# Performance work log

Measured on AMD Instinct MI355X. Metric: run time of the kernel, lower is better.

## Reference

```python
import jax, jax.numpy as jnp
import numpy as np

D = 64            # node_out_feats
G = 1000          # number of graphs in batch
NPG = 32          # nodes per graph
N = G * NPG       # total nodes = 32000
E = 80000         # total edges
NODE_IN = 74
EDGE_IN = 12
EH = 128          # edge_hidden_feats
STEPS_MP = 6
STEPS_S2S = 6
LSTM_LAYERS = 3
N_TASKS = 1


def setup_inputs() -> dict:
    key = jax.random.key(0)
    ks = jax.random.split(key, 32)

    def lin(k, fi, fo):
        return (jax.random.normal(k, (fi, fo), jnp.float32) / np.float32(np.sqrt(fi)))

    # edges constrained within graphs
    eg = jax.random.randint(ks[0], (E,), 0, G)
    inp = {
        "node_feats": jax.random.normal(ks[1], (N, NODE_IN), jnp.float32),
        "edge_feats": jax.random.normal(ks[2], (E, EDGE_IN), jnp.float32),
        "src": (eg * NPG + jax.random.randint(ks[3], (E,), 0, NPG)).astype(jnp.int32),
        "dst": (eg * NPG + jax.random.randint(ks[4], (E,), 0, NPG)).astype(jnp.int32),
        "segment_ids": (jnp.arange(N, dtype=jnp.int32) // NPG),
        "Wp": lin(ks[5], NODE_IN, D), "bp": jnp.zeros((D,), jnp.float32),
        "We1": lin(ks[6], EDGE_IN, EH), "be1": jnp.zeros((EH,), jnp.float32),
        "We2": lin(ks[7], EH, D * D), "be2": jnp.zeros((D * D,), jnp.float32),
        "b_conv": jnp.zeros((D,), jnp.float32),
        "gru_Wx": lin(ks[8], D, 3 * D), "gru_Wh": lin(ks[9], D, 3 * D),
        "gru_bx": jnp.zeros((3 * D,), jnp.float32), "gru_bh": jnp.zeros((3 * D,), jnp.float32),
        "Wout1": lin(ks[10], 2 * D, D), "bout1": jnp.zeros((D,), jnp.float32),
        "Wout2": lin(ks[11], D, N_TASKS), "bout2": jnp.zeros((N_TASKS,), jnp.float32),
    }
    for l in range(LSTM_LAYERS):
        fi = 2 * D if l == 0 else D
        inp[f"lstm_Wx{l}"] = lin(ks[12 + 4 * l], fi, 4 * D)
        inp[f"lstm_Wh{l}"] = lin(ks[13 + 4 * l], D, 4 * D)
        inp[f"lstm_bx{l}"] = jnp.zeros((4 * D,), jnp.float32)
        inp[f"lstm_bh{l}"] = jnp.zeros((4 * D,), jnp.float32)
    return inp


def reference(node_feats, edge_feats, src, dst, segment_ids,
              Wp, bp, We1, be1, We2, be2, b_conv,
              gru_Wx, gru_Wh, gru_bx, gru_bh,
              Wout1, bout1, Wout2, bout2,
              lstm_Wx0, lstm_Wh0, lstm_bx0, lstm_bh0,
              lstm_Wx1, lstm_Wh1, lstm_bx1, lstm_bh1,
              lstm_Wx2, lstm_Wh2, lstm_bx2, lstm_bh2):
    # ---- MPNNGNN ----
    h = jax.nn.relu(node_feats @ Wp + bp)                 # [N, D]
    hidden = h                                            # GRU hidden state
    # edge network -> per-edge [D, D] weight matrix (edge feats are constant,
    # so compute once; DGL recomputes each step with identical result)
    W_edge = (jax.nn.relu(edge_feats @ We1 + be1) @ We2 + be2).reshape(E, D, D)
    for _ in range(STEPS_MP):
        msg = jnp.einsum('ed,edo->eo', h[src], W_edge)    # [E, D] per-edge matvec
        agg = jax.ops.segment_sum(msg, dst, num_segments=N) + b_conv
        x = jax.nn.relu(agg)
        # GRU cell (torch gate order r, z, n)
        gx = x @ gru_Wx + gru_bx
        gh = hidden @ gru_Wh + gru_bh
        r = jax.nn.sigmoid(gx[:, :D] + gh[:, :D])
        z = jax.nn.sigmoid(gx[:, D:2 * D] + gh[:, D:2 * D])
        n = jnp.tanh(gx[:, 2 * D:] + r * gh[:, 2 * D:])
        hidden = (1.0 - z) * n + z * hidden
        h = hidden
    # ---- Set2Set readout ----
    lstm = [(lstm_Wx0, lstm_Wh0, lstm_bx0, lstm_bh0),
            (lstm_Wx1, lstm_Wh1, lstm_bx1, lstm_bh1),
            (lstm_Wx2, lstm_Wh2, lstm_bx2, lstm_bh2)]
    hs = [jnp.zeros((G, D), h.dtype) for _ in range(LSTM_LAYERS)]
    cs = [jnp.zeros((G, D), h.dtype) for _ in range(LSTM_LAYERS)]
    q_star = jnp.zeros((G, 2 * D), h.dtype)
    for _ in range(STEPS_S2S):
        xq = q_star
        for l, (Wx, Wh, bx, bh) in enumerate(lstm):
            gates = xq @ Wx + bx + hs[l] @ Wh + bh        # [G, 4D], torch order i,f,g,o
            i, f, g_, o = jnp.split(gates, 4, axis=-1)
            c = jax.nn.sigmoid(f) * cs[l] + jax.nn.sigmoid(i) * jnp.tanh(g_)
            hs[l] = jax.nn.sigmoid(o) * jnp.tanh(c)
            cs[l] = c
            xq = hs[l]
        q = xq                                            # [G, D]
        e = jnp.sum(h * q[segment_ids], axis=-1)          # [N] attention logits
        emax = jax.ops.segment_max(e, segment_ids, num_segments=G)
        ee = jnp.exp(e - emax[segment_ids])
        alpha = ee / jax.ops.segment_sum(ee, segment_ids, num_segments=G)[segment_ids]
        readout = jax.ops.segment_sum(h * alpha[:, None], segment_ids, num_segments=G)
        q_star = jnp.concatenate([q, readout], axis=-1)   # [G, 2D]
    # ---- prediction head ----
    pred = jax.nn.relu(q_star @ Wout1 + bout1) @ Wout2 + bout2
    return pred, q_star
```

## Files before the change

kernel.cpp:

```cpp
#include <hip/hip_runtime.h>

typedef __attribute__((ext_vector_type(8))) _Float16 f16x8;
typedef __attribute__((ext_vector_type(2))) _Float16 f16x2;
typedef __attribute__((ext_vector_type(4))) float floatx4;

union HFrag { uint4 u4; f16x8 v; unsigned short s[8]; };
union HS { _Float16 h; unsigned short u; };
union UH2 { unsigned int u; f16x2 h; };

__device__ __forceinline__ float bf2f(unsigned short u) {
  return __uint_as_float(((unsigned int)u) << 16);
}
__device__ __forceinline__ float h2f(unsigned short u) { HS z; z.u = u; return (float)z.h; }
__device__ __forceinline__ unsigned short f2h(float f) { HS z; z.h = (_Float16)f; return z.u; }
__device__ __forceinline__ float sigmf(float x) { return 1.0f / (1.0f + expf(-x)); }

__device__ __forceinline__ float ldi(const void* p, long i, bool f32) {
  return f32 ? ((const float*)p)[i] : bf2f(((const unsigned short*)p)[i]);
}

__device__ __forceinline__ void dma16(unsigned short* lds, const unsigned short* g) {
  __builtin_amdgcn_global_load_lds(
      (const __attribute__((address_space(1))) unsigned int*)g,
      (__attribute__((address_space(3))) unsigned int*)lds,
      16, 0, 0);
}

#define WAIT_VM5()   __builtin_amdgcn_s_waitcnt(0x0F75)
#define WAIT_VM0()   __builtin_amdgcn_s_waitcnt(0x0F70)
#define WAIT_LGKM0() __builtin_amdgcn_s_waitcnt(0xC07F)

#define SAFE_BARRIER() do {                      \
  __builtin_amdgcn_sched_barrier(0);             \
  WAIT_LGKM0();                                  \
  __builtin_amdgcn_s_barrier();                  \
  __builtin_amdgcn_sched_barrier(0);             \
} while (0)

#define NNODES 32000
#define NEDGES 80000
#define NGRAPH 1000

#define MFMA_F16 __builtin_amdgcn_mfma_f32_16x16x32_f16

__global__ __launch_bounds__(256) void detect_kernel(
    const unsigned short* __restrict__ nf, int* __restrict__ flag) {
  __shared__ float sm[256];
  float m = 0.f;
  for (int i = threadIdx.x; i < 4096; i += 256) {
    float v = fabsf(bf2f(nf[i]));
    if (isfinite(v)) m = fmaxf(m, v);
    else m = 1e30f;
  }
  sm[threadIdx.x] = m;
  __syncthreads();
  if (threadIdx.x == 0) {
    float mm = 0.f;
    for (int i = 0; i < 256; ++i) mm = fmaxf(mm, sm[i]);
    flag[0] = (mm > 1e6f) ? 1 : 0;
  }
}

__global__ __launch_bounds__(256) void prep_kernel(
    const int* __restrict__ dflag,
    const void* __restrict__ Wx, const void* __restrict__ Wh,
    const void* __restrict__ bx, const void* __restrict__ bh,
    const void* __restrict__ bconv,
    unsigned short* __restrict__ WxH, unsigned short* __restrict__ WhH,
    float* __restrict__ bxf, float* __restrict__ bhf, float* __restrict__ bconvf) {
  bool f32 = dflag[0] != 0;
  int idx = blockIdx.x * 256 + threadIdx.x;
  int j = idx >> 6, k = idx & 63;
  WxH[idx] = f2h(ldi(Wx, k * 192 + j, f32));
  WhH[idx] = f2h(ldi(Wh, k * 192 + j, f32));
  if (idx < 192) { bxf[idx] = ldi(bx, idx, f32); bhf[idx] = ldi(bh, idx, f32); }
  if (idx < 64) bconvf[idx] = ldi(bconv, idx, f32);
}

__global__ __launch_bounds__(256) void lstmprep_kernel(
    const int* __restrict__ dflag,
    const void* Wx0, const void* Wh0, const void* bx0, const void* bh0,
    const void* Wx1, const void* Wh1, const void* bx1, const void* bh1,
    const void* Wx2, const void* Wh2, const void* bx2, const void* bh2,
    float4* __restrict__ LW, float* __restrict__ bsum) {
  bool f32 = dflag[0] != 0;
  int idx = blockIdx.x * 256 + threadIdx.x;
  int l, base, fi;
  if (idx < 12288)      { l = 0; base = 0;     fi = 128; }
  else if (idx < 20480) { l = 1; base = 12288; fi = 64; }
  else                  { l = 2; base = 20480; fi = 64; }
  const void* Wx = (l == 0) ? Wx0 : (l == 1) ? Wx1 : Wx2;
  const void* Wh = (l == 0) ? Wh0 : (l == 1) ? Wh1 : Wh2;
  int r = idx - base;
  int c = r >> 8, t = r & 255;
  float v[4];
#pragma unroll
  for (int i2 = 0; i2 < 4; ++i2) {
    int k = c * 4 + i2;
    v[i2] = (k < fi) ? ldi(Wx, (long)k * 256 + t, f32)
                     : ldi(Wh, (long)(k - fi) * 256 + t, f32);
  }
  float4 o; o.x = v[0]; o.y = v[1]; o.z = v[2]; o.w = v[3];
  LW[idx] = o;
  if (idx < 768) {
    int ll = idx >> 8, j = idx & 255;
    const void* bx = (ll == 0) ? bx0 : (ll == 1) ? bx1 : bx2;
    const void* bh = (ll == 0) ? bh0 : (ll == 1) ? bh1 : bh2;
    bsum[idx] = ldi(bx, j, f32) + ldi(bh, j, f32);
  }
}

__global__ __launch_bounds__(256) void nodeproj_kernel(
    const int* __restrict__ dflag,
    const void* __restrict__ nf, const void* __restrict__ Wp,
    const void* __restrict__ bp, float* __restrict__ hstate) {
  bool f32 = dflag[0] != 0;
  int lane = threadIdx.x & 63;
  int n = blockIdx.x * 4 + (threadIdx.x >> 6);
  float acc = ldi(bp, lane, f32);
  for (int k = 0; k < 74; ++k)
    acc += ldi(nf, (long)n * 74 + k, f32) * ldi(Wp, k * 64 + lane, f32);
  hstate[n * 64 + lane] = fmaxf(acc, 0.0f);
}

__global__ __launch_bounds__(256) void we2t_kernel(
    const int* __restrict__ dflag,
    const void* __restrict__ We2, unsigned short* __restrict__ We2T) {
  bool f32 = dflag[0] != 0;
  int idx = blockIdx.x * 256 + threadIdx.x;
  int j = idx & 7;
  int gs = (idx >> 3) & 7;
  int o = (idx >> 6) & 63;
  int k = idx >> 12;
  int g = gs ^ (o & 7);
  int d = g * 8 + j;
  We2T[idx] = f2h(ldi(We2, (long)k * 4096 + d * 64 + o, f32));
}

__global__ __launch_bounds__(256) void be2t_kernel(
    const int* __restrict__ dflag,
    const void* __restrict__ be2, unsigned short* __restrict__ be2T) {
  bool f32 = dflag[0] != 0;
  int idx = blockIdx.x * 256 + threadIdx.x;
  int j = idx & 7;
  int gs = (idx >> 3) & 7;
  int o = idx >> 6;
  int g = gs ^ (o & 7);
  int d = g * 8 + j;
  be2T[idx] = f2h(ldi(be2, (long)d * 64 + o, f32));
}

__global__ __launch_bounds__(256) void count_kernel(
    const int* __restrict__ dst, int* __restrict__ cnt) {
  int e = blockIdx.x * 256 + threadIdx.x;
  if (e < NEDGES) atomicAdd(&cnt[dst[e]], 1);
}

__global__ __launch_bounds__(256) void scan_kernel(
    const int* __restrict__ cnt, int* __restrict__ row_ptr, int* __restrict__ cur) {
  __shared__ int part[256];
  int t = threadIdx.x;
  int base = t * 125;
  int s = 0;
  for (int i = 0; i < 125; ++i) s += cnt[base + i];
  part[t] = s;
  __syncthreads();
  if (t == 0) {
    int run = 0;
    for (int i = 0; i < 256; ++i) { int v = part[i]; part[i] = run; run += v; }
  }
  __syncthreads();
  int run = part[t];
  for (int i = 0; i < 125; ++i) {
    row_ptr[base + i] = run;
    cur[base + i] = run;
    run += cnt[base + i];
  }
  if (t == 255) row_ptr[32000] = run;
}

__global__ __launch_bounds__(256) void fill_kernel(
    const int* __restrict__ dst, int* __restrict__ cur, int* __restrict__ eidx) {
  int e = blockIdx.x * 256 + threadIdx.x;
  if (e < NEDGES) { int p = atomicAdd(&cur[dst[e]], 1); eidx[p] = e; }
}

__global__ __launch_bounds__(256) void uprep_kernel(
    const int* __restrict__ dflag,
    const void* __restrict__ ef, const void* __restrict__ We1,
    const void* __restrict__ be1, const int* __restrict__ eidx,
    unsigned int* __restrict__ uT) {
  bool f32 = dflag[0] != 0;
  __shared__ float we1_s[1536];
  __shared__ float be1_s[128];
  int t = threadIdx.x;
  for (int i = t; i < 1536; i += 256) we1_s[i] = ldi(We1, i, f32);
  if (t < 128) be1_s[t] = ldi(be1, t, f32);
  __syncthreads();
  int pos = blockIdx.x * 256 + t;
  if (pos >= NEDGES) return;
  int e = eidx[pos];
  float efr[12];
#pragma unroll
  for (int j = 0; j < 12; ++j) efr[j] = ldi(ef, (long)e * 12 + j, f32);
#pragma unroll 4
  for (int kp = 0; kp < 64; ++kp) {
    int k0 = kp * 2;
    float u0 = be1_s[k0], u1 = be1_s[k0 + 1];
#pragma unroll
    for (int j = 0; j < 12; ++j) {
      u0 += efr[j] * we1_s[j * 128 + k0];
      u1 += efr[j] * we1_s[j * 128 + k0 + 1];
    }
    u0 = fmaxf(u0, 0.f); u1 = fmaxf(u1, 0.f);
    HS a, b; a.h = (_Float16)u0; b.h = (_Float16)u1;
    uT[(size_t)kp * NEDGES + pos] = (unsigned int)a.u | ((unsigned int)b.u << 16);
  }
}

__device__ __forceinline__ void issueB(unsigned short* L, const unsigned short* G,
                                       int w, int lane) {
  L += w * 1024; G += w * 1024 + lane * 8;
  dma16(L, G); dma16(L + 512, G + 512);
  dma16(L + 4096, G + 4096); dma16(L + 4096 + 512, G + 4096 + 512);
}

__device__ __forceinline__ void zchunk(
    unsigned short (*BtL)[8192], unsigned int (*Zs)[64][68],
    const HFrag (&bhi)[4][2], const HFrag (&blo)[4][2],
    int arow, int g0q, int g1q, int c16, int w, int q,
    int cb, int zc, bool act, int r, unsigned int ucur, floatx4 (&msgv)[16]) {
  HFrag a00, a01, a10, a11;
  a00.u4 = *(const uint4*)&BtL[cb][arow + g0q];
  a01.u4 = *(const uint4*)&BtL[cb][arow + g1q];
  a10.u4 = *(const uint4*)&BtL[cb][4096 + arow + g0q];
  a11.u4 = *(const uint4*)&BtL[cb][4096 + arow + g1q];
  __builtin_amdgcn_sched_barrier(0);
  WAIT_LGKM0();
  __builtin_amdgcn_sched_barrier(0);
  floatx4 z0[4], z1[4];
#pragma unroll
  for (int nt = 0; nt < 4; ++nt) {
    z0[nt] = (floatx4){0.f, 0.f, 0.f, 0.f};
    z1[nt] = (floatx4){0.f, 0.f, 0.f, 0.f};
  }
#pragma unroll
  for (int nt = 0; nt < 4; ++nt) {
    z0[nt] = MFMA_F16(a00.v, bhi[nt][0].v, z0[nt], 0, 0, 0);
    z0[nt] = MFMA_F16(a00.v, blo[nt][0].v, z0[nt], 0, 0, 0);
    z0[nt] = MFMA_F16(a01.v, bhi[nt][1].v, z0[nt], 0, 0, 0);
    z0[nt] = MFMA_F16(a01.v, blo[nt][1].v, z0[nt], 0, 0, 0);
    z1[nt] = MFMA_F16(a10.v, bhi[nt][0].v, z1[nt], 0, 0, 0);
    z1[nt] = MFMA_F16(a10.v, blo[nt][0].v, z1[nt], 0, 0, 0);
    z1[nt] = MFMA_F16(a11.v, bhi[nt][1].v, z1[nt], 0, 0, 0);
    z1[nt] = MFMA_F16(a11.v, blo[nt][1].v, z1[nt], 0, 0, 0);
  }
#pragma unroll
  for (int nt = 0; nt < 4; ++nt) {
    uint4 st;
    HS p0h, p1h;
    p0h.h = (_Float16)z0[nt][0]; p1h.h = (_Float16)z1[nt][0];
    st.x = (unsigned int)p0h.u | ((unsigned int)p1h.u << 16);
    p0h.h = (_Float16)z0[nt][1]; p1h.h = (_Float16)z1[nt][1];
    st.y = (unsigned int)p0h.u | ((unsigned int)p1h.u << 16);
    p0h.h = (_Float16)z0[nt][2]; p1h.h = (_Float16)z1[nt][2];
    st.z = (unsigned int)p0h.u | ((unsigned int)p1h.u << 16);
    p0h.h = (_Float16)z0[nt][3]; p1h.h = (_Float16)z1[nt][3];
    st.w = (unsigned int)p0h.u | ((unsigned int)p1h.u << 16);
    *(uint4*)&Zs[zc][nt * 16 + c16][w * 16 + q * 4] = st;
  }
  SAFE_BARRIER();
  if (act) {
    UH2 uu; uu.u = ucur;
#pragma unroll
    for (int og = 0; og < 16; ++og) {
      uint4 zz = *(const uint4*)&Zs[zc][r][og * 4];
      UH2 a;
      a.u = zz.x; msgv[og][0] = __builtin_amdgcn_fdot2(a.h, uu.h, msgv[og][0], false);
      a.u = zz.y; msgv[og][1] = __builtin_amdgcn_fdot2(a.h, uu.h, msgv[og][1], false);
      a.u = zz.z; msgv[og][2] = __builtin_amdgcn_fdot2(a.h, uu.h, msgv[og][2], false);
      a.u = zz.w; msgv[og][3] = __builtin_amdgcn_fdot2(a.h, uu.h, msgv[og][3], false);
    }
  }
}

__global__ __launch_bounds__(256, 2) void step_fused_kernel(
    const unsigned short* __restrict__ We2T,
    const unsigned short* __restrict__ be2T,
    const unsigned int* __restrict__ uT,
    const int* __restrict__ src, const int* __restrict__ eidx,
    const int* __restrict__ row_ptr,
    const unsigned short* __restrict__ WxH, const unsigned short* __restrict__ WhH,
    const float* __restrict__ bxf, const float* __restrict__ bhf,
    const float* __restrict__ bconvf,
    float* __restrict__ hstate) {
  __shared__ __align__(16) unsigned char RA[67584];
  unsigned short (*BtL)[8192] = (unsigned short (*)[8192])RA;
  unsigned int (*Zs)[64][68] = (unsigned int (*)[64][68])(RA + 32768);
  float (*MS)[64] = (float (*)[64])RA;
  unsigned short (*Xhi)[72] = (unsigned short (*)[72])RA;
  unsigned short (*Xlo)[72] = (unsigned short (*)[72])(RA + 9216);
  unsigned short (*SRZ)[65] = (unsigned short (*)[65])(RA + 18432);
  float (*NG)[65] = (float (*)[65])(RA + 35072);

  int t = threadIdx.x, lane = t & 63, w = t >> 6;
  int c16 = lane & 15, q = lane >> 4;
  int nb = blockIdx.x * 64;
  int p0 = row_ptr[nb], p1 = row_ptr[nb + 64];
  int nE = p1 - p0;

  HFrag bhi[4][2], blo[4][2];
#pragma unroll
  for (int nt = 0; nt < 4; ++nt)
#pragma unroll
    for (int ks = 0; ks < 2; ++ks) {
      const float* hp = hstate + (size_t)(nb + nt * 16 + c16) * 64 + ks * 32 + q * 8;
      float4 v0 = *(const float4*)hp;
      float4 v1 = *(const float4*)(hp + 4);
      float vv[8] = {v0.x, v0.y, v0.z, v0.w, v1.x, v1.y, v1.z, v1.w};
#pragma unroll
      for (int j = 0; j < 8; ++j) {
        HS hi; hi.h = (_Float16)vv[j];
        bhi[nt][ks].s[j] = hi.u;
        blo[nt][ks].s[j] = f2h(vv[j] - (float)hi.h);
      }
    }

  int arow = (w * 16 + c16) * 64;
  int g0q = (q ^ (c16 & 7)) * 8;
  int g1q = ((4 + q) ^ (c16 & 7)) * 8;

  float aggv[16];
  {
    float bcv = bconvf[lane];
#pragma unroll
    for (int i = 0; i < 16; ++i) aggv[i] = bcv;
  }

  for (int et = 0; et < nE; et += 256) {
    int me = et + t;
    bool act = me < nE;
    int pos = p0 + (act ? me : 0);
    int r = src[eidx[pos]] - nb;

    unsigned int uA = uT[pos];
    dma16(&BtL[0][0] + w * 1024, be2T + w * 1024 + lane * 8);
    dma16(&BtL[0][0] + w * 1024 + 512, be2T + w * 1024 + 512 + lane * 8);
    issueB(&BtL[1][0], We2T, w, lane);
    WAIT_VM0();

    floatx4 hacc[4];
#pragma unroll
    for (int nt = 0; nt < 4; ++nt) hacc[nt] = (floatx4){0.f, 0.f, 0.f, 0.f};
    {
      HFrag aB0, aB1;
      aB0.u4 = *(const uint4*)&BtL[0][arow + g0q];
      aB1.u4 = *(const uint4*)&BtL[0][arow + g1q];
#pragma unroll
      for (int nt = 0; nt < 4; ++nt) {
        hacc[nt] = MFMA_F16(aB0.v, bhi[nt][0].v, hacc[nt], 0, 0, 0);
        hacc[nt] = MFMA_F16(aB0.v, blo[nt][0].v, hacc[nt], 0, 0, 0);
        hacc[nt] = MFMA_F16(aB1.v, bhi[nt][1].v, hacc[nt], 0, 0, 0);
        hacc[nt] = MFMA_F16(aB1.v, blo[nt][1].v, hacc[nt], 0, 0, 0);
      }
    }
    __builtin_amdgcn_sched_barrier(0);
    WAIT_LGKM0();
    __builtin_amdgcn_sched_barrier(0);
    unsigned int uB = uT[(size_t)NEDGES + pos];
    issueB(&BtL[0][0], We2T + 8192, w, lane);
#pragma unroll
    for (int nt = 0; nt < 4; ++nt)
      *(floatx4*)&Zs[1][nt * 16 + c16][w * 16 + q * 4] = hacc[nt];
    SAFE_BARRIER();

    floatx4 msgv[16];
    if (act) {
#pragma unroll
      for (int og = 0; og < 16; ++og)
        msgv[og] = *(const floatx4*)&Zs[1][r][og * 4];
    }

    for (int cc = 0; cc < 32; ++cc) {
      const int c0 = cc * 2;
      WAIT_VM5();
      zchunk(BtL, Zs, bhi, blo, arow, g0q, g1q, c16, w, q, 1, 0, act, r, uA, msgv);
      if (c0 + 2 < 64) {
        __builtin_amdgcn_sched_barrier(0);
        uA = uT[(size_t)(c0 + 2) * NEDGES + pos];
        issueB(&BtL[1][0], We2T + (size_t)(c0 + 2) * 8192, w, lane);
      }
      if (c0 + 1 == 63) WAIT_VM0(); else WAIT_VM5();
      zchunk(BtL, Zs, bhi, blo, arow, g0q, g1q, c16, w, q, 0, 1, act, r, uB, msgv);
      if (c0 + 3 < 64) {
        __builtin_amdgcn_sched_barrier(0);
        uB = uT[(size_t)(c0 + 3) * NEDGES + pos];
        issueB(&BtL[0][0], We2T + (size_t)(c0 + 3) * 8192, w, lane);
      }
    }

    __syncthreads();
    if (act) {
      int t7 = t & 7;
#pragma unroll
      for (int og = 0; og < 16; ++og)
        *(floatx4*)&MS[t][(og ^ t7) * 4] = msgv[og];
    }
    __syncthreads();
    {
      int nT = nE - et; if (nT > 256) nT = 256;
      int c = t & 63;
      int cq = c >> 2, cj = c & 3;
#pragma unroll
      for (int i = 0; i < 16; ++i) {
        int node = nb + (t >> 6) + i * 4;
        int rs = row_ptr[node] - p0 - et;
        int re = row_ptr[node + 1] - p0 - et;
        int lo = rs < 0 ? 0 : rs;
        int hi = re > nT ? nT : re;
        float a = aggv[i];
        for (int p = lo; p < hi; ++p)
          a += MS[p][((cq ^ (p & 7)) << 2) | cj];
        aggv[i] = a;
      }
    }
    __syncthreads();
  }

#pragma unroll
  for (int i = 0; i < 16; ++i) {
    int n = (t >> 6) + i * 4;
    int c = t & 63;
    float x = fmaxf(aggv[i], 0.f);
    HS hx; hx.h = (_Float16)x;
    Xhi[n][c] = hx.u;
    Xlo[n][c] = f2h(x - (float)hx.h);
  }
  __syncthreads();

  floatx4 gx[3][4], gh[3][4];
#pragma unroll
  for (int jt = 0; jt < 3; ++jt)
#pragma unroll
    for (int nt = 0; nt < 4; ++nt) {
      gx[jt][nt] = (floatx4){0.f, 0.f, 0.f, 0.f};
      gh[jt][nt] = (floatx4){0.f, 0.f, 0.f, 0.f};
    }
#pragma unroll
  for (int kc = 0; kc < 2; ++kc) {
    int kof = kc * 32 + q * 8;
    HFrag ax[3], ah[3];
#pragma unroll
    for (int jt = 0; jt < 3; ++jt) {
      long off = (long)((w * 3 + jt) * 16 + c16) * 64 + kof;
      ax[jt].u4 = *(const uint4*)(WxH + off);
      ah[jt].u4 = *(const uint4*)(WhH + off);
    }
    HFrag bxh[4], bxl[4];
#pragma unroll
    for (int nt = 0; nt < 4; ++nt) {
      int n = nt * 16 + c16;
      bxh[nt].u4 = *(const uint4*)&Xhi[n][kof];
      bxl[nt].u4 = *(const uint4*)&Xlo[n][kof];
    }
#pragma unroll
    for (int jt = 0; jt < 3; ++jt)
#pragma unroll
      for (int nt = 0; nt < 4; ++nt) {
        gx[jt][nt] = MFMA_F16(ax[jt].v, bxh[nt].v, gx[jt][nt], 0, 0, 0);
        gx[jt][nt] = MFMA_F16(ax[jt].v, bxl[nt].v, gx[jt][nt], 0, 0, 0);
        gh[jt][nt] = MFMA_F16(ah[jt].v, bhi[nt][kc].v, gh[jt][nt], 0, 0, 0);
      }
  }

#pragma unroll
  for (int jt = 0; jt < 3; ++jt) {
#pragma unroll
    for (int rr = 0; rr < 4; ++rr) {
      int j = (w * 3 + jt) * 16 + q * 4 + rr;
      float bxv = bxf[j], bhv = bhf[j];
#pragma unroll
      for (int nt = 0; nt < 4; ++nt) {
        float vx = gx[jt][nt][rr] + bxv;
        float vh = gh[jt][nt][rr] + bhv;
        if (j < 128) {
          SRZ[j][nt * 16 + c16] = f2h(sigmf(vx + vh));
        } else {
          gx[jt][nt][rr] = vx;
          gh[jt][nt][rr] = vh;
        }
      }
    }
  }
  __syncthreads();

#pragma unroll
  for (int jt = 0; jt < 3; ++jt) {
#pragma unroll
    for (int rr = 0; rr < 4; ++rr) {
      int j = (w * 3 + jt) * 16 + q * 4 + rr;
      if (j >= 128) {
        int f = j - 128;
#pragma unroll
        for (int nt = 0; nt < 4; ++nt) {
          int n = nt * 16 + c16;
          float rg = h2f(SRZ[f][n]);
          NG[f][n] = tanhf(gx[jt][nt][rr] + rg * gh[jt][nt][rr]);
        }
      }
    }
  }
  __syncthreads();

#pragma unroll
  for (int i = 0; i < 16; ++i) {
    int n = (t >> 6) + i * 4;
    int f = t & 63;
    float z = h2f(SRZ[64 + f][n]);
    float ng = NG[f][n];
    size_t gi = (size_t)(nb + n) * 64 + f;
    float ho = hstate[gi];
    hstate[gi] = (1.0f - z) * ng + z * ho;
  }
}

__global__ __launch_bounds__(512) void s2s6_kernel(
    const int* __restrict__ dflag,
    const float* __restrict__ hstate,
    const float4* __restrict__ LW,
    const float* __restrict__ lstm_bsum,
    const void* __restrict__ Wout1, const void* __restrict__ bout1,
    const void* __restrict__ Wout2, const void* __restrict__ bout2,
    float* __restrict__ out) {
  bool f32 = dflag[0] != 0;
  __shared__ float xq[2][128];
  __shared__ float inb[2][192];
  __shared__ float gates[2][256];
  __shared__ float al[2][32];
  __shared__ float hsvf[384];
  __shared__ float csvf[384];
  int g0 = blockIdx.x * 2;
  int t = threadIdx.x;

  for (int i = t; i < 256; i += 512) xq[i >> 7][i & 127] = 0.f;
  for (int i = t; i < 384; i += 512) { hsvf[i] = 0.f; csvf[i] = 0.f; }
  __syncthreads();

  int tt = t & 255, gp = t >> 8;

  for (int s = 0; s < 6; ++s) {
#pragma unroll
    for (int l = 0; l < 3; ++l) {
      const int fi = (l == 0) ? 128 : 64;
      const int tot = fi + 64;
      for (int i = t; i < 2 * tot; i += 512) {
        int g = i / tot, k = i - g * tot;
        inb[g][k] = (k < fi) ? xq[g][k] : hsvf[l * 128 + g * 64 + (k - fi)];
      }
      __syncthreads();
      const int nch = tot >> 2;
      const float4* wrow = LW + ((l == 0) ? 0 : (l == 1) ? 12288 : 20480) + tt;
      float bs = lstm_bsum[l * 256 + tt];
      float a0 = bs;
#pragma unroll 8
      for (int cch = 0; cch < nch; ++cch) {
        float4 wv = wrow[(size_t)cch * 256];
        float4 x0 = *(const float4*)&inb[gp][cch * 4];
        a0 += wv.x * x0.x + wv.y * x0.y + wv.z * x0.z + wv.w * x0.w;
      }
      gates[gp][tt] = a0;
      __syncthreads();
      if (t < 128) {
        int gg = t >> 6, u = t & 63;
        float ig = sigmf(gates[gg][u]);
        float fg = sigmf(gates[gg][64 + u]);
        float gv = tanhf(gates[gg][128 + u]);
        float og = sigmf(gates[gg][192 + u]);
        int ci = l * 128 + t;
        float cc = fg * csvf[ci] + ig * gv;
        float hn = og * tanhf(cc);
        csvf[ci] = cc;
        hsvf[ci] = hn;
        xq[gg][u] = hn;
      }
      __syncthreads();
    }
    if (t < 128) {
      int gg = t >> 6, tl = t & 63;
      int g = g0 + gg;
      int n = tl & 31, half = tl >> 5;
      const float* hrow = hstate + (size_t)(g * 32 + n) * 64 + half * 32;
      const float* qp = &xq[gg][half * 32];
      float p = 0.f;
#pragma unroll
      for (int k = 0; k < 32; ++k) p += hrow[k] * qp[k];
      p += __shfl_xor(p, 32, 64);
      if (half == 0) {
        float m = p;
#pragma unroll
        for (int s2 = 1; s2 < 32; s2 <<= 1) m = fmaxf(m, __shfl_xor(m, s2, 32));
        float e = expf(p - m);
        float sum = e;
#pragma unroll
        for (int s2 = 1; s2 < 32; s2 <<= 1) sum += __shfl_xor(sum, s2, 32);
        al[gg][n] = e / sum;
      }
      float acc = 0.f;
#pragma unroll 8
      for (int nn = 0; nn < 32; ++nn)
        acc += al[gg][nn] * hstate[(size_t)(g * 32 + nn) * 64 + tl];
      xq[gg][64 + tl] = acc;
    }
    __syncthreads();
  }

  if (t < 128) {
    int gg = t >> 6, tl = t & 63;
    int g = g0 + gg;
    float acc = ldi(bout1, tl, f32);
#pragma unroll 16
    for (int k = 0; k < 128; ++k) acc += xq[gg][k] * ldi(Wout1, k * 64 + tl, f32);
    acc = fmaxf(acc, 0.0f);
    float p = acc * ldi(Wout2, tl, f32);
#pragma unroll
    for (int m = 1; m < 64; m <<= 1) p += __shfl_xor(p, m, 64);
    if (tl == 0) out[g] = p + ldi(bout2, 0, f32);
    out[1000 + g * 128 + tl] = xq[gg][tl];
    out[1000 + g * 128 + 64 + tl] = xq[gg][64 + tl];
  }
}

extern "C" void kernel_launch(void* const* d_in, const int* in_sizes, int n_in,
                              void* d_out, int out_size, void* d_ws, size_t ws_size,
                              hipStream_t stream) {
  (void)in_sizes; (void)n_in; (void)out_size; (void)ws_size;
  const void* node_feats = d_in[0];
  const void* edge_feats = d_in[1];
  const int* src = (const int*)d_in[2];
  const int* dst = (const int*)d_in[3];
  const void* Wp = d_in[5];
  const void* bp = d_in[6];
  const void* We1 = d_in[7];
  const void* be1 = d_in[8];
  const void* We2 = d_in[9];
  const void* be2 = d_in[10];
  const void* b_conv = d_in[11];
  const void* gWx = d_in[12];
  const void* gWh = d_in[13];
  const void* gbx = d_in[14];
  const void* gbh = d_in[15];
  const void* Wout1 = d_in[16];
  const void* bout1 = d_in[17];
  const void* Wout2 = d_in[18];
  const void* bout2 = d_in[19];

  int* dflag = (int*)d_ws;
  float* hstate = (float*)d_ws + 64;
  unsigned int* uT = (unsigned int*)(hstate + NNODES * 64);
  unsigned short* We2T = (unsigned short*)(uT + (size_t)NEDGES * 64);
  unsigned short* WxH = We2T + 524288;
  unsigned short* WhH = WxH + 12288;
  float* bxf = (float*)(WhH + 12288);
  float* bhf = bxf + 192;
  float* bconvf = bhf + 192;
  int* row_ptr = (int*)(bconvf + 64);
  int* cur = row_ptr + 32001;
  int* cnt = cur + 32000;
  int* eidx = cnt + 32000;
  uintptr_t lwp = (uintptr_t)(eidx + 80000);
  lwp = (lwp + 15) & ~(uintptr_t)15;
  float4* LWf = (float4*)lwp;
  float* lstm_bsum = (float*)(LWf + 28672);
  unsigned short* be2T = (unsigned short*)(lstm_bsum + 768);

  (void)hipMemsetAsync(cnt, 0, (size_t)NNODES * sizeof(int), stream);

  detect_kernel<<<1, 256, 0, stream>>>((const unsigned short*)node_feats, dflag);
  prep_kernel<<<48, 256, 0, stream>>>(dflag, gWx, gWh, gbx, gbh, b_conv,
                                      WxH, WhH, bxf, bhf, bconvf);
  nodeproj_kernel<<<NNODES / 4, 256, 0, stream>>>(dflag, node_feats, Wp, bp, hstate);
  we2t_kernel<<<2048, 256, 0, stream>>>(dflag, We2, We2T);
  be2t_kernel<<<16, 256, 0, stream>>>(dflag, be2, be2T);
  lstmprep_kernel<<<112, 256, 0, stream>>>(dflag,
      d_in[20], d_in[21], d_in[22], d_in[23],
      d_in[24], d_in[25], d_in[26], d_in[27],
      d_in[28], d_in[29], d_in[30], d_in[31],
      LWf, lstm_bsum);

  count_kernel<<<(NEDGES + 255) / 256, 256, 0, stream>>>(dst, cnt);
  scan_kernel<<<1, 256, 0, stream>>>(cnt, row_ptr, cur);
  fill_kernel<<<(NEDGES + 255) / 256, 256, 0, stream>>>(dst, cur, eidx);
  uprep_kernel<<<(NEDGES + 255) / 256, 256, 0, stream>>>(
      dflag, edge_feats, We1, be1, eidx, uT);

  for (int step = 0; step < 6; ++step) {
    step_fused_kernel<<<NNODES / 64, 256, 0, stream>>>(
        We2T, be2T, uT, src, eidx, row_ptr, WxH, WhH, bxf, bhf, bconvf, hstate);
  }
  s2s6_kernel<<<NGRAPH / 2, 512, 0, stream>>>(dflag, hstate,
      (const float4*)LWf, lstm_bsum,
      Wout1, bout1, Wout2, bout2, (float*)d_out);
}
```

Baseline: 1.097 ms.

## Single-buffer We2 chunks and halve MS staging to fit three blocks per CU

Replaces the double-buffered We2T chunk pipeline with one LDS buffer. Each chunk's fragments are read into registers before the next chunk's DMA is issued. The message staging buffer is split into two 128-edge halves, which cuts the shared-memory footprint from about 66KB to about 51KB, and launch bounds are raised to 3 blocks per CU. The aim is higher occupancy to hide latency, at the cost of exposing the full global-load latency each chunk (wait on vmcnt 0), extra barriers, and tighter register limits.

```diff
diff --git a/kernel.cpp b/kernel.cpp
--- a/kernel.cpp
+++ b/kernel.cpp
@@ -26,7 +26,6 @@
       16, 0, 0);
 }
 
-#define WAIT_VM5()   __builtin_amdgcn_s_waitcnt(0x0F75)
 #define WAIT_VM0()   __builtin_amdgcn_s_waitcnt(0x0F70)
 #define WAIT_LGKM0() __builtin_amdgcn_s_waitcnt(0xC07F)
 
@@ -225,66 +224,7 @@
   dma16(L + 4096, G + 4096); dma16(L + 4096 + 512, G + 4096 + 512);
 }
 
-__device__ __forceinline__ void zchunk(
-    unsigned short (*BtL)[8192], unsigned int (*Zs)[64][68],
-    const HFrag (&bhi)[4][2], const HFrag (&blo)[4][2],
-    int arow, int g0q, int g1q, int c16, int w, int q,
-    int cb, int zc, bool act, int r, unsigned int ucur, floatx4 (&msgv)[16]) {
-  HFrag a00, a01, a10, a11;
-  a00.u4 = *(const uint4*)&BtL[cb][arow + g0q];
-  a01.u4 = *(const uint4*)&BtL[cb][arow + g1q];
-  a10.u4 = *(const uint4*)&BtL[cb][4096 + arow + g0q];
-  a11.u4 = *(const uint4*)&BtL[cb][4096 + arow + g1q];
-  __builtin_amdgcn_sched_barrier(0);
-  WAIT_LGKM0();
-  __builtin_amdgcn_sched_barrier(0);
-  floatx4 z0[4], z1[4];
-#pragma unroll
-  for (int nt = 0; nt < 4; ++nt) {
-    z0[nt] = (floatx4){0.f, 0.f, 0.f, 0.f};
-    z1[nt] = (floatx4){0.f, 0.f, 0.f, 0.f};
-  }
-#pragma unroll
-  for (int nt = 0; nt < 4; ++nt) {
-    z0[nt] = MFMA_F16(a00.v, bhi[nt][0].v, z0[nt], 0, 0, 0);
-    z0[nt] = MFMA_F16(a00.v, blo[nt][0].v, z0[nt], 0, 0, 0);
-    z0[nt] = MFMA_F16(a01.v, bhi[nt][1].v, z0[nt], 0, 0, 0);
-    z0[nt] = MFMA_F16(a01.v, blo[nt][1].v, z0[nt], 0, 0, 0);
-    z1[nt] = MFMA_F16(a10.v, bhi[nt][0].v, z1[nt], 0, 0, 0);
-    z1[nt] = MFMA_F16(a10.v, blo[nt][0].v, z1[nt], 0, 0, 0);
-    z1[nt] = MFMA_F16(a11.v, bhi[nt][1].v, z1[nt], 0, 0, 0);
-    z1[nt] = MFMA_F16(a11.v, blo[nt][1].v, z1[nt], 0, 0, 0);
-  }
-#pragma unroll
-  for (int nt = 0; nt < 4; ++nt) {
-    uint4 st;
-    HS p0h, p1h;
-    p0h.h = (_Float16)z0[nt][0]; p1h.h = (_Float16)z1[nt][0];
-    st.x = (unsigned int)p0h.u | ((unsigned int)p1h.u << 16);
-    p0h.h = (_Float16)z0[nt][1]; p1h.h = (_Float16)z1[nt][1];
-    st.y = (unsigned int)p0h.u | ((unsigned int)p1h.u << 16);
-    p0h.h = (_Float16)z0[nt][2]; p1h.h = (_Float16)z1[nt][2];
-    st.z = (unsigned int)p0h.u | ((unsigned int)p1h.u << 16);
-    p0h.h = (_Float16)z0[nt][3]; p1h.h = (_Float16)z1[nt][3];
-    st.w = (unsigned int)p0h.u | ((unsigned int)p1h.u << 16);
-    *(uint4*)&Zs[zc][nt * 16 + c16][w * 16 + q * 4] = st;
-  }
-  SAFE_BARRIER();
-  if (act) {
-    UH2 uu; uu.u = ucur;
-#pragma unroll
-    for (int og = 0; og < 16; ++og) {
-      uint4 zz = *(const uint4*)&Zs[zc][r][og * 4];
-      UH2 a;
-      a.u = zz.x; msgv[og][0] = __builtin_amdgcn_fdot2(a.h, uu.h, msgv[og][0], false);
-      a.u = zz.y; msgv[og][1] = __builtin_amdgcn_fdot2(a.h, uu.h, msgv[og][1], false);
-      a.u = zz.z; msgv[og][2] = __builtin_amdgcn_fdot2(a.h, uu.h, msgv[og][2], false);
-      a.u = zz.w; msgv[og][3] = __builtin_amdgcn_fdot2(a.h, uu.h, msgv[og][3], false);
-    }
-  }
-}
-
-__global__ __launch_bounds__(256, 2) void step_fused_kernel(
+__global__ __launch_bounds__(256, 3) void step_fused_kernel(
     const unsigned short* __restrict__ We2T,
     const unsigned short* __restrict__ be2T,
     const unsigned int* __restrict__ uT,
@@ -294,9 +234,9 @@
     const float* __restrict__ bxf, const float* __restrict__ bhf,
     const float* __restrict__ bconvf,
     float* __restrict__ hstate) {
-  __shared__ __align__(16) unsigned char RA[67584];
-  unsigned short (*BtL)[8192] = (unsigned short (*)[8192])RA;
-  unsigned int (*Zs)[64][68] = (unsigned int (*)[64][68])(RA + 32768);
+  __shared__ __align__(16) unsigned char RA[51712];
+  unsigned short* BtL = (unsigned short*)RA;
+  unsigned int (*Zs)[64][68] = (unsigned int (*)[64][68])(RA + 16384);
   float (*MS)[64] = (float (*)[64])RA;
   unsigned short (*Xhi)[72] = (unsigned short (*)[72])RA;
   unsigned short (*Xlo)[72] = (unsigned short (*)[72])(RA + 9216);
@@ -343,32 +283,29 @@
     int pos = p0 + (act ? me : 0);
     int r = src[eidx[pos]] - nb;
 
-    unsigned int uA = uT[pos];
-    dma16(&BtL[0][0] + w * 1024, be2T + w * 1024 + lane * 8);
-    dma16(&BtL[0][0] + w * 1024 + 512, be2T + w * 1024 + 512 + lane * 8);
-    issueB(&BtL[1][0], We2T, w, lane);
+    unsigned int ucur = uT[pos];
+    dma16(BtL + w * 1024, be2T + w * 1024 + lane * 8);
+    dma16(BtL + w * 1024 + 512, be2T + w * 1024 + 512 + lane * 8);
     WAIT_VM0();
 
-    floatx4 hacc[4];
-#pragma unroll
-    for (int nt = 0; nt < 4; ++nt) hacc[nt] = (floatx4){0.f, 0.f, 0.f, 0.f};
-    {
-      HFrag aB0, aB1;
-      aB0.u4 = *(const uint4*)&BtL[0][arow + g0q];
-      aB1.u4 = *(const uint4*)&BtL[0][arow + g1q];
-#pragma unroll
-      for (int nt = 0; nt < 4; ++nt) {
-        hacc[nt] = MFMA_F16(aB0.v, bhi[nt][0].v, hacc[nt], 0, 0, 0);
-        hacc[nt] = MFMA_F16(aB0.v, blo[nt][0].v, hacc[nt], 0, 0, 0);
-        hacc[nt] = MFMA_F16(aB1.v, bhi[nt][1].v, hacc[nt], 0, 0, 0);
-        hacc[nt] = MFMA_F16(aB1.v, blo[nt][1].v, hacc[nt], 0, 0, 0);
-      }
-    }
+    HFrag eb0, eb1;
+    eb0.u4 = *(const uint4*)&BtL[arow + g0q];
+    eb1.u4 = *(const uint4*)&BtL[arow + g1q];
     __builtin_amdgcn_sched_barrier(0);
     WAIT_LGKM0();
     __builtin_amdgcn_sched_barrier(0);
-    unsigned int uB = uT[(size_t)NEDGES + pos];
-    issueB(&BtL[0][0], We2T + 8192, w, lane);
+    issueB(BtL, We2T, w, lane);
+
+    floatx4 hacc[4];
+#pragma unroll
+    for (int nt = 0; nt < 4; ++nt) hacc[nt] = (floatx4){0.f, 0.f, 0.f, 0.f};
+#pragma unroll
+    for (int nt = 0; nt < 4; ++nt) {
+      hacc[nt] = MFMA_F16(eb0.v, bhi[nt][0].v, hacc[nt], 0, 0, 0);
+      hacc[nt] = MFMA_F16(eb0.v, blo[nt][0].v, hacc[nt], 0, 0, 0);
+      hacc[nt] = MFMA_F16(eb1.v, bhi[nt][1].v, hacc[nt], 0, 0, 0);
+      hacc[nt] = MFMA_F16(eb1.v, blo[nt][1].v, hacc[nt], 0, 0, 0);
+    }
 #pragma unroll
     for (int nt = 0; nt < 4; ++nt)
       *(floatx4*)&Zs[1][nt * 16 + c16][w * 16 + q * 4] = hacc[nt];
@@ -381,26 +318,75 @@
         msgv[og] = *(const floatx4*)&Zs[1][r][og * 4];
     }
 
-    for (int cc = 0; cc < 32; ++cc) {
-      const int c0 = cc * 2;
-      WAIT_VM5();
-      zchunk(BtL, Zs, bhi, blo, arow, g0q, g1q, c16, w, q, 1, 0, act, r, uA, msgv);
-      if (c0 + 2 < 64) {
-        __builtin_amdgcn_sched_barrier(0);
-        uA = uT[(size_t)(c0 + 2) * NEDGES + pos];
-        issueB(&BtL[1][0], We2T + (size_t)(c0 + 2) * 8192, w, lane);
-      }
-      if (c0 + 1 == 63) WAIT_VM0(); else WAIT_VM5();
-      zchunk(BtL, Zs, bhi, blo, arow, g0q, g1q, c16, w, q, 0, 1, act, r, uB, msgv);
-      if (c0 + 3 < 64) {
-        __builtin_amdgcn_sched_barrier(0);
-        uB = uT[(size_t)(c0 + 3) * NEDGES + pos];
-        issueB(&BtL[0][0], We2T + (size_t)(c0 + 3) * 8192, w, lane);
-      }
+    for (int c = 0; c < 64; ++c) {
+      WAIT_VM0();
+      HFrag a00, a01, a10, a11;
+      a00.u4 = *(const uint4*)&BtL[arow + g0q];
+      a01.u4 = *(const uint4*)&BtL[arow + g1q];
+      a10.u4 = *(const uint4*)&BtL[4096 + arow + g0q];
+      a11.u4 = *(const uint4*)&BtL[4096 + arow + g1q];
+      __builtin_amdgcn_sched_barrier(0);
+      WAIT_LGKM0();
+      __builtin_amdgcn_sched_barrier(0);
+      unsigned int unext = 0;
+      if (c + 1 < 64) {
+        unext = uT[(size_t)(c + 1) * NEDGES + pos];
+        issueB(BtL, We2T + (size_t)(c + 1) * 8192, w, lane);
+      }
+      floatx4 z0[4], z1[4];
+#pragma unroll
+      for (int nt = 0; nt < 4; ++nt) {
+        z0[nt] = (floatx4){0.f, 0.f, 0.f, 0.f};
+        z1[nt] = (floatx4){0.f, 0.f, 0.f, 0.f};
+      }
+#pragma unroll
+      for (int nt = 0; nt < 4; ++nt) {
+        z0[nt] = MFMA_F16(a00.v, bhi[nt][0].v, z0[nt], 0, 0, 0);
+        z0[nt] = MFMA_F16(a00.v, blo[nt][0].v, z0[nt], 0, 0, 0);
+        z0[nt] = MFMA_F16(a01.v, bhi[nt][1].v, z0[nt], 0, 0, 0);
+        z0[nt] = MFMA_F16(a01.v, blo[nt][1].v, z0[nt], 0, 0, 0);
+        z1[nt] = MFMA_F16(a10.v, bhi[nt][0].v, z1[nt], 0, 0, 0);
+        z1[nt] = MFMA_F16(a10.v, blo[nt][0].v, z1[nt], 0, 0, 0);
+        z1[nt] = MFMA_F16(a11.v, bhi[nt][1].v, z1[nt], 0, 0, 0);
+        z1[nt] = MFMA_F16(a11.v, blo[nt][1].v, z1[nt], 0, 0, 0);
+      }
+      int zc = c & 1;
+#pragma unroll
+      for (int nt = 0; nt < 4; ++nt) {
+        uint4 st;
+        HS ph0, ph1;
+        ph0.h = (_Float16)z0[nt][0]; ph1.h = (_Float16)z1[nt][0];
+        st.x = (unsigned int)ph0.u | ((unsigned int)ph1.u << 16);
+        ph0.h = (_Float16)z0[nt][1]; ph1.h = (_Float16)z1[nt][1];
+        st.y = (unsigned int)ph0.u | ((unsigned int)ph1.u << 16);
+        ph0.h = (_Float16)z0[nt][2]; ph1.h = (_Float16)z1[nt][2];
+        st.z = (unsigned int)ph0.u | ((unsigned int)ph1.u << 16);
+        ph0.h = (_Float16)z0[nt][3]; ph1.h = (_Float16)z1[nt][3];
+        st.w = (unsigned int)ph0.u | ((unsigned int)ph1.u << 16);
+        *(uint4*)&Zs[zc][nt * 16 + c16][w * 16 + q * 4] = st;
+      }
+      SAFE_BARRIER();
+
+      if (act) {
+        UH2 uu; uu.u = ucur;
+#pragma unroll
+        for (int og = 0; og < 16; ++og) {
+          uint4 zz = *(const uint4*)&Zs[zc][r][og * 4];
+          UH2 a;
+          a.u = zz.x; msgv[og][0] = __builtin_amdgcn_fdot2(a.h, uu.h, msgv[og][0], false);
+          a.u = zz.y; msgv[og][1] = __builtin_amdgcn_fdot2(a.h, uu.h, msgv[og][1], false);
+          a.u = zz.z; msgv[og][2] = __builtin_amdgcn_fdot2(a.h, uu.h, msgv[og][2], false);
+          a.u = zz.w; msgv[og][3] = __builtin_amdgcn_fdot2(a.h, uu.h, msgv[og][3], false);
+        }
+      }
+      ucur = unext;
     }
 
     __syncthreads();
-    if (act) {
+    int nT = nE - et; if (nT > 256) nT = 256;
+    int cgi = t & 63;
+    int cq = cgi >> 2, cj = cgi & 3;
+    if (act && t < 128) {
       int t7 = t & 7;
 #pragma unroll
       for (int og = 0; og < 16; ++og)
@@ -408,19 +394,39 @@
     }
     __syncthreads();
     {
-      int nT = nE - et; if (nT > 256) nT = 256;
-      int c = t & 63;
-      int cq = c >> 2, cj = c & 3;
+      int nA = nT < 128 ? nT : 128;
 #pragma unroll
       for (int i = 0; i < 16; ++i) {
         int node = nb + (t >> 6) + i * 4;
         int rs = row_ptr[node] - p0 - et;
         int re = row_ptr[node + 1] - p0 - et;
         int lo = rs < 0 ? 0 : rs;
+        int hi = re > nA ? nA : re;
+        float a = aggv[i];
+        for (int p = lo; p < hi; ++p)
+          a += MS[p][((cq ^ (p & 7)) << 2) | cj];
+        aggv[i] = a;
+      }
+    }
+    __syncthreads();
+    if (act && t >= 128) {
+      int t7 = t & 7;
+#pragma unroll
+      for (int og = 0; og < 16; ++og)
+        *(floatx4*)&MS[t - 128][(og ^ t7) * 4] = msgv[og];
+    }
+    __syncthreads();
+    {
+#pragma unroll
+      for (int i = 0; i < 16; ++i) {
+        int node = nb + (t >> 6) + i * 4;
+        int rs = row_ptr[node] - p0 - et;
+        int re = row_ptr[node + 1] - p0 - et;
+        int lo = rs < 128 ? 128 : rs;
         int hi = re > nT ? nT : re;
         float a = aggv[i];
         for (int p = lo; p < hi; ++p)
-          a += MS[p][((cq ^ (p & 7)) << 2) | cj];
+          a += MS[p - 128][((cq ^ (p & 7)) << 2) | cj];
         aggv[i] = a;
       }
     }
```

New measurement: 1.799 ms. 1.64x slower.
